# Performance work log

Measured on AMD Instinct MI355X. Metric: run time of the kernel, lower is better.

The kernel has to match this reference:

```python
import jax, jax.numpy as jnp
import numpy as np

BSZ, N, DEG = 32, 128, 8
HID, NODE_F, EDGE_F = 64, 32, 16
E_PER_G = N * DEG
E_TOT = BSZ * E_PER_G
N_TOT = BSZ * N


def _edges():
    # ring-style unique edges per graph: (i, (i+d) % N) for d in 1..DEG
    i = np.repeat(np.arange(N), DEG)              # [N*DEG]
    d = np.tile(np.arange(1, DEG + 1), N)
    src_l = np.tile(i, BSZ)                       # local src per edge
    dst_l = np.tile((i + d) % N, BSZ)
    off = np.repeat(np.arange(BSZ) * N, E_PER_G)
    ei = np.stack([src_l + off, dst_l + off])     # [2, E_TOT] global
    return jnp.asarray(ei, jnp.int32)


def setup_inputs() -> dict:
    key = jax.random.key(0)
    ks = jax.random.split(key, 16)
    def lin(k, fi, fo):
        s = 1.0 / np.sqrt(fi)
        kw, kb = jax.random.split(k)
        return (jax.random.uniform(kw, (fi, fo), jnp.float32, -s, s),
                jax.random.uniform(kb, (fo,), jnp.float32, -s, s))
    W_atom, b_atom = lin(ks[0], NODE_F, HID)
    W_bond, b_bond = lin(ks[1], EDGE_F, HID)
    be_w1, be_b1 = lin(ks[2], HID, HID)   # GINE bond_encoder MLP
    be_w2, be_b2 = lin(ks[3], HID, HID)
    nn_w1, nn_b1 = lin(ks[4], HID, HID)   # GINE update seq
    nn_w2, nn_b2 = lin(ks[5], HID, HID)
    m_w1, m_b1 = lin(ks[6], 2 * HID, HID) # final MLP: outer(HID)+edge(HID) -> HID -> 1
    m_w2, m_b2 = lin(ks[7], HID, 1)
    return {
        "x": jax.random.normal(ks[8], (N_TOT, NODE_F), jnp.float32),
        "edge_attr": jax.random.normal(ks[9], (E_TOT, EDGE_F), jnp.float32),
        "edge_index": _edges(),
        "batch": jnp.repeat(jnp.arange(BSZ, dtype=jnp.int32), N),
        "W_atom": W_atom, "b_atom": b_atom, "W_bond": W_bond, "b_bond": b_bond,
        "be_w1": be_w1, "be_b1": be_b1, "be_w2": be_w2, "be_b2": be_b2,
        "nn_w1": nn_w1, "nn_b1": nn_b1, "nn_w2": nn_w2, "nn_b2": nn_b2,
        "m_w1": m_w1, "m_b1": m_b1, "m_w2": m_w2, "m_b2": m_b2,
    }


def reference(x, edge_attr, edge_index, batch,
              W_atom, b_atom, W_bond, b_bond,
              be_w1, be_b1, be_w2, be_b2,
              nn_w1, nn_b1, nn_w2, nn_b2,
              m_w1, m_b1, m_w2, m_b2):
    src, dst = edge_index[0], edge_index[1]
    h = x @ W_atom + b_atom                                   # atom encoder [N_TOT, HID]
    e = edge_attr @ W_bond + b_bond                           # bond encoder [E_TOT, HID]
    # --- GINEConv (eps=0): nn(h + sum_j relu(h_j + mlp(e_ij))) ---
    ee = jax.nn.relu(e @ be_w1 + be_b1) @ be_w2 + be_b2
    msg = jax.nn.relu(h[src] + ee)
    agg = jax.ops.segment_sum(msg, dst, num_segments=N_TOT)
    h = jax.nn.relu((h + agg) @ nn_w1 + nn_b1) @ nn_w2 + nn_b2
    # --- dense batch (equal-size graphs -> exact reshape) ---
    logits = h.reshape(BSZ, N, HID)
    real_mask = jnp.ones((BSZ, N, N), dtype=bool)
    # --- outer pairwise tuples ---
    outer = jnp.einsum('bnk,bmk->bnmk', logits, logits)       # [B,N,N,HID]
    # --- scatter edge embeddings into dense [B,N,N,HID] ---
    g = src // N
    ls, ld = src % N, dst % N
    dense_e = jnp.zeros((BSZ, N, N, HID), e.dtype).at[g, ls, ld].set(e)
    emb = jnp.concatenate([outer, dense_e], axis=-1)          # [B,N,N,2*HID]
    emb = jax.nn.relu(emb @ m_w1 + m_b1) @ m_w2 + m_b2        # [B,N,N,1]
    return emb, real_mask
```

## Files before the change

kernel.cpp:

```cpp
#include <hip/hip_runtime.h>

#define BSZ 32
#define NN 128
#define DEG 8
#define HID 64
#define NODE_F 32
#define EDGE_F 16
#define E_PER_G (NN * DEG)
#define E_TOT (BSZ * E_PER_G)
#define N_TOT (BSZ * NN)
#define EMB_SIZE (BSZ * NN * NN)

typedef __attribute__((ext_vector_type(8))) short short8;
typedef __attribute__((ext_vector_type(4))) float f32x4;

__device__ __forceinline__ unsigned short f2bf(float f) {
    unsigned u = __builtin_bit_cast(unsigned, f);
    u += 0x7FFF + ((u >> 16) & 1);
    return (unsigned short)(u >> 16);
}
__device__ __forceinline__ float bf2f(unsigned short s) {
    unsigned u = ((unsigned)s) << 16;
    return __builtin_bit_cast(float, u);
}
__device__ __forceinline__ int lds_b(int row, int col) {
    return row * 128 + (((col >> 3) ^ (row & 7)) << 4) + ((col & 7) << 1);
}
__device__ __forceinline__ int lds_c(int row, int c8) {
    return row * 128 + ((c8 ^ (row & 7)) << 4);
}

__global__ __launch_bounds__(256) void k_pre(const float* __restrict__ x,
        const float* __restrict__ W_atom, const float* __restrict__ b_atom,
        const float* __restrict__ W_bond, const float* __restrict__ be_w1,
        const float* __restrict__ be_w2, const float* __restrict__ m_w1,
        const float* __restrict__ nn_w1, const float* __restrict__ nn_w2,
        float* __restrict__ h, unsigned short* __restrict__ PK,
        unsigned short* __restrict__ W1T) {
    int tid = threadIdx.x;
    if (blockIdx.x < 256) {
        __shared__ float xs[16][NODE_F];
        int i2 = tid * 2;
        float2 v = *(const float2*)&x[(size_t)blockIdx.x * 16 * NODE_F + i2];
        xs[i2 >> 5][i2 & 31] = v.x;
        xs[i2 >> 5][(i2 & 31) + 1] = v.y;
        int j = tid & 63, q = tid >> 6;
        float ww[NODE_F];
#pragma unroll
        for (int k = 0; k < NODE_F; ++k) ww[k] = W_atom[k * HID + j];
        float bj = b_atom[j];
        __syncthreads();
#pragma unroll
        for (int r = 0; r < 4; ++r) {
            int row = q * 4 + r;
            float acc = bj;
#pragma unroll
            for (int k = 0; k < NODE_F; ++k) acc = fmaf(xs[row][k], ww[k], acc);
            h[(size_t)(blockIdx.x * 16 + row) * HID + j] = acc;
        }
    } else {
        int t = (blockIdx.x - 256) * 256 + tid;
        int m = t >> 12;
        int idx = t & 4095;
        if (m < 6) {
            int i = idx & 7, lr = (idx >> 3) & 15, lg = (idx >> 7) & 3;
            int jt = (idx >> 9) & 3, kh = (idx >> 11) & 1;
            int k = kh * 32 + lg * 8 + i, j = jt * 16 + lr;
            float v;
            switch (m) {
                case 0:  v = (k < EDGE_F) ? W_bond[k * HID + j] : 0.f; break;
                case 1:  v = be_w1[k * HID + j]; break;
                case 2:  v = be_w2[k * HID + j]; break;
                case 3:  v = m_w1[(HID + k) * HID + j]; break;
                case 4:  v = nn_w1[k * HID + j]; break;
                default: v = nn_w2[k * HID + j]; break;
            }
            PK[m * 4096 + idx] = f2bf(v);
        } else {
            int j = idx >> 6, k = idx & 63;
            W1T[idx] = f2bf(m_w1[k * HID + j]);
        }
    }
}

__global__ __launch_bounds__(256) void k_edgeM(
        const float* __restrict__ ea, const float* __restrict__ h,
        const float* __restrict__ b_bond, const float* __restrict__ be_b1,
        const float* __restrict__ be_b2, const unsigned short* __restrict__ PK,
        float* __restrict__ E1, unsigned short* __restrict__ msgb) {
    __shared__ char ebuf[64 * 128];
    __shared__ char tbuf[64 * 128];
    int tid = threadIdx.x;
    int w = tid >> 6, l = tid & 63, lr = l & 15, lg = l >> 4;
    int e0 = blockIdx.x * 64;
    int R0 = w * 16;

    short8 af = (short8){0, 0, 0, 0, 0, 0, 0, 0};
    if (lg < 2) {
        const float* p = ea + (size_t)(e0 + R0 + lr) * EDGE_F + lg * 8;
        float4 x0 = *(const float4*)p;
        float4 x1 = *(const float4*)(p + 4);
        af[0] = (short)f2bf(x0.x); af[1] = (short)f2bf(x0.y);
        af[2] = (short)f2bf(x0.z); af[3] = (short)f2bf(x0.w);
        af[4] = (short)f2bf(x1.x); af[5] = (short)f2bf(x1.y);
        af[6] = (short)f2bf(x1.z); af[7] = (short)f2bf(x1.w);
    }
    f32x4 a0[4];
#pragma unroll
    for (int jt = 0; jt < 4; ++jt) a0[jt] = (f32x4){0.f, 0.f, 0.f, 0.f};
#pragma unroll
    for (int jt = 0; jt < 4; ++jt) {
        short8 bw = *(const short8*)(PK + 0 * 4096 + (size_t)(((0 * 4 + jt) * 4 + lg) * 16 + lr) * 8);
        a0[jt] = __builtin_amdgcn_mfma_f32_16x16x32_bf16(af, bw, a0[jt], 0, 0, 0);
    }
#pragma unroll
    for (int jt = 0; jt < 4; ++jt) {
        float bb = b_bond[jt * 16 + lr];
#pragma unroll
        for (int r = 0; r < 4; ++r) {
            int row = R0 + lg * 4 + r, col = jt * 16 + lr;
            *(unsigned short*)(ebuf + lds_b(row, col)) = f2bf(a0[jt][r] + bb);
        }
    }
    short8 ae[2];
#pragma unroll
    for (int kh = 0; kh < 2; ++kh)
        ae[kh] = *(const short8*)(ebuf + lds_c(R0 + lr, kh * 4 + lg));
    f32x4 a1[4];
#pragma unroll
    for (int jt = 0; jt < 4; ++jt) a1[jt] = (f32x4){0.f, 0.f, 0.f, 0.f};
#pragma unroll
    for (int kh = 0; kh < 2; ++kh)
#pragma unroll
        for (int jt = 0; jt < 4; ++jt) {
            short8 bw = *(const short8*)(PK + 3 * 4096 + (size_t)(((kh * 4 + jt) * 4 + lg) * 16 + lr) * 8);
            a1[jt] = __builtin_amdgcn_mfma_f32_16x16x32_bf16(ae[kh], bw, a1[jt], 0, 0, 0);
        }
#pragma unroll
    for (int jt = 0; jt < 4; ++jt)
        *(f32x4*)(E1 + (size_t)(e0 + R0) * HID + jt * 256 + l * 4) = a1[jt];
    f32x4 a2[4];
#pragma unroll
    for (int jt = 0; jt < 4; ++jt) a2[jt] = (f32x4){0.f, 0.f, 0.f, 0.f};
#pragma unroll
    for (int kh = 0; kh < 2; ++kh)
#pragma unroll
        for (int jt = 0; jt < 4; ++jt) {
            short8 bw = *(const short8*)(PK + 1 * 4096 + (size_t)(((kh * 4 + jt) * 4 + lg) * 16 + lr) * 8);
            a2[jt] = __builtin_amdgcn_mfma_f32_16x16x32_bf16(ae[kh], bw, a2[jt], 0, 0, 0);
        }
#pragma unroll
    for (int jt = 0; jt < 4; ++jt) {
        float b1j = be_b1[jt * 16 + lr];
#pragma unroll
        for (int r = 0; r < 4; ++r) {
            int row = R0 + lg * 4 + r, col = jt * 16 + lr;
            *(unsigned short*)(tbuf + lds_b(row, col)) = f2bf(fmaxf(a2[jt][r] + b1j, 0.f));
        }
    }
    short8 at[2];
#pragma unroll
    for (int kh = 0; kh < 2; ++kh)
        at[kh] = *(const short8*)(tbuf + lds_c(R0 + lr, kh * 4 + lg));
    f32x4 a3[4];
#pragma unroll
    for (int jt = 0; jt < 4; ++jt) a3[jt] = (f32x4){0.f, 0.f, 0.f, 0.f};
#pragma unroll
    for (int kh = 0; kh < 2; ++kh)
#pragma unroll
        for (int jt = 0; jt < 4; ++jt) {
            short8 bw = *(const short8*)(PK + 2 * 4096 + (size_t)(((kh * 4 + jt) * 4 + lg) * 16 + lr) * 8);
            a3[jt] = __builtin_amdgcn_mfma_f32_16x16x32_bf16(at[kh], bw, a3[jt], 0, 0, 0);
        }
    int g = e0 >> 10;
#pragma unroll
    for (int jt = 0; jt < 4; ++jt) {
        float b2j = be_b2[jt * 16 + lr];
#pragma unroll
        for (int r = 0; r < 4; ++r) {
            int row = R0 + lg * 4 + r;
            int ig = (e0 & 1023) + row;
            int src = g * NN + (ig >> 3);
            float hv = h[(size_t)src * HID + jt * 16 + lr];
            float mv = fmaxf(hv + a3[jt][r] + b2j, 0.f);
            msgb[(size_t)(e0 + row) * HID + jt * 16 + lr] = f2bf(mv);
        }
    }
}

__global__ __launch_bounds__(128) void k_nodeM(
        const float* __restrict__ h, const unsigned short* __restrict__ msgb,
        const float* __restrict__ nb1, const float* __restrict__ nb2,
        const unsigned short* __restrict__ PK, unsigned short* __restrict__ Lbf) {
    __shared__ char ub[16 * 128];
    __shared__ char tb[16 * 128];
    int tid = threadIdx.x;
    int n0 = blockIdx.x * 16;
    int g = n0 >> 7, nl0 = n0 & 127;
    {
        int r = tid >> 3;
        int c0 = (tid & 7) * 8;
        int nl = nl0 + r;
        float u[8];
        float4 h0 = *(const float4*)&h[(size_t)(n0 + r) * HID + c0];
        float4 h1 = *(const float4*)&h[(size_t)(n0 + r) * HID + c0 + 4];
        u[0] = h0.x; u[1] = h0.y; u[2] = h0.z; u[3] = h0.w;
        u[4] = h1.x; u[5] = h1.y; u[6] = h1.z; u[7] = h1.w;
#pragma unroll
        for (int d = 1; d <= 8; ++d) {
            int eid = g * E_PER_G + ((nl - d) & 127) * DEG + (d - 1);
            uint4 mv = *(const uint4*)&msgb[(size_t)eid * HID + c0];
            unsigned wd[4] = {mv.x, mv.y, mv.z, mv.w};
#pragma unroll
            for (int q = 0; q < 4; ++q) {
                u[q * 2]     += bf2f((unsigned short)(wd[q] & 0xffff));
                u[q * 2 + 1] += bf2f((unsigned short)(wd[q] >> 16));
            }
        }
        uint4 pk;
        pk.x = (unsigned)f2bf(u[0]) | ((unsigned)f2bf(u[1]) << 16);
        pk.y = (unsigned)f2bf(u[2]) | ((unsigned)f2bf(u[3]) << 16);
        pk.z = (unsigned)f2bf(u[4]) | ((unsigned)f2bf(u[5]) << 16);
        pk.w = (unsigned)f2bf(u[6]) | ((unsigned)f2bf(u[7]) << 16);
        *(uint4*)(ub + lds_c(r, tid & 7)) = pk;
    }
    __syncthreads();
    int w = tid >> 6, l = tid & 63, lr = l & 15, lg = l >> 4;
    short8 au[2];
#pragma unroll
    for (int kh = 0; kh < 2; ++kh)
        au[kh] = *(const short8*)(ub + lds_c(lr, kh * 4 + lg));
    f32x4 a1[2];
#pragma unroll
    for (int q = 0; q < 2; ++q) a1[q] = (f32x4){0.f, 0.f, 0.f, 0.f};
#pragma unroll
    for (int q = 0; q < 2; ++q) {
        int jt = w * 2 + q;
#pragma unroll
        for (int kh = 0; kh < 2; ++kh) {
            short8 bw = *(const short8*)(PK + 4 * 4096 + (size_t)(((kh * 4 + jt) * 4 + lg) * 16 + lr) * 8);
            a1[q] = __builtin_amdgcn_mfma_f32_16x16x32_bf16(au[kh], bw, a1[q], 0, 0, 0);
        }
    }
#pragma unroll
    for (int q = 0; q < 2; ++q) {
        int jt = w * 2 + q;
        float b1j = nb1[jt * 16 + lr];
#pragma unroll
        for (int r = 0; r < 4; ++r) {
            int row = lg * 4 + r, col = jt * 16 + lr;
            *(unsigned short*)(tb + lds_b(row, col)) = f2bf(fmaxf(a1[q][r] + b1j, 0.f));
        }
    }
    __syncthreads();
    short8 at[2];
#pragma unroll
    for (int kh = 0; kh < 2; ++kh)
        at[kh] = *(const short8*)(tb + lds_c(lr, kh * 4 + lg));
    f32x4 a2[2];
#pragma unroll
    for (int q = 0; q < 2; ++q) a2[q] = (f32x4){0.f, 0.f, 0.f, 0.f};
#pragma unroll
    for (int q = 0; q < 2; ++q) {
        int jt = w * 2 + q;
#pragma unroll
        for (int kh = 0; kh < 2; ++kh) {
            short8 bw = *(const short8*)(PK + 5 * 4096 + (size_t)(((kh * 4 + jt) * 4 + lg) * 16 + lr) * 8);
            a2[q] = __builtin_amdgcn_mfma_f32_16x16x32_bf16(at[kh], bw, a2[q], 0, 0, 0);
        }
    }
#pragma unroll
    for (int q = 0; q < 2; ++q) {
        int jt = w * 2 + q;
        float b2j = nb2[jt * 16 + lr];
#pragma unroll
        for (int r = 0; r < 4; ++r) {
            int row = lg * 4 + r;
            Lbf[(size_t)(n0 + row) * HID + jt * 16 + lr] = f2bf(a2[q][r] + b2j);
        }
    }
}

__global__ __launch_bounds__(256, 4) void k_pair(
        const unsigned short* __restrict__ Lbf, const float* __restrict__ E1,
        const unsigned short* __restrict__ W1T,
        const float* __restrict__ m_b1, const float* __restrict__ m_w2,
        const float* __restrict__ m_b2, float* __restrict__ out,
        float* __restrict__ mask, int write_mask) {
    __shared__ uint4 Ls[1024];
    __shared__ float eseg[1024];
    int tid = threadIdx.x;
    int bid = (blockIdx.x & 7) * 256 + (blockIdx.x >> 3);
    int b = bid >> 6;
    int nb = (bid & 63) * 2;
    if (write_mask && tid < 64) {
        *(float4*)(mask + (size_t)(b * NN + nb) * NN + tid * 4) =
            make_float4(1.f, 1.f, 1.f, 1.f);
    }
    const uint4* src = (const uint4*)(Lbf + (size_t)b * NN * HID);
#pragma unroll
    for (int it = 0; it < 4; ++it) {
        int i = it * 256 + tid;
        int row = i >> 3, c = i & 7;
        Ls[(row << 3) | (c ^ (row & 7))] = src[i];
    }
    ((float4*)eseg)[tid] = ((const float4*)(E1 + (size_t)(b * E_PER_G + nb * DEG) * HID))[tid];

    int w = tid >> 6, l = tid & 63, lr = l & 15, lg = l >> 4;
    int n = nb + (w >> 1);
    int hm = (w & 1) * 64;
    const unsigned short* LnG = Lbf + (size_t)(b * NN + n) * HID;
    short8 an[2][4];
#pragma unroll
    for (int kh = 0; kh < 2; ++kh) {
        short8 lnc = *(const short8*)(LnG + kh * 32 + lg * 8);
        float lf[8];
#pragma unroll
        for (int i = 0; i < 8; ++i) lf[i] = bf2f((unsigned short)lnc[i]);
#pragma unroll
        for (int jt = 0; jt < 4; ++jt) {
            short8 w1t = *(const short8*)(W1T + (size_t)(jt * 16 + lr) * HID + kh * 32 + lg * 8);
#pragma unroll
            for (int i = 0; i < 8; ++i)
                an[kh][jt][i] = (short)f2bf(lf[i] * bf2f((unsigned short)w1t[i]));
        }
    }
    float4 b1v[4], w2v[4];
#pragma unroll
    for (int jt = 0; jt < 4; ++jt) {
        b1v[jt] = *(const float4*)&m_b1[jt * 16 + lg * 4];
        w2v[jt] = *(const float4*)&m_w2[jt * 16 + lg * 4];
    }
    float bias2 = m_b2[0];
    __syncthreads();

    const unsigned short* Lsu = (const unsigned short*)Ls;
    float* orow = out + ((size_t)(b * NN + n)) * NN;
#pragma unroll
    for (int mt = 0; mt < 4; ++mt) {
        int row = hm + mt * 16 + lr;
        f32x4 acc[4];
#pragma unroll
        for (int jt = 0; jt < 4; ++jt) acc[jt] = (f32x4){0.f, 0.f, 0.f, 0.f};
#pragma unroll
        for (int kh = 0; kh < 2; ++kh) {
            int c = kh * 4 + lg;
            short8 afr = *(const short8*)(Lsu + (size_t)((row << 3) | (c ^ (row & 7))) * 8);
#pragma unroll
            for (int jt = 0; jt < 4; ++jt)
                acc[jt] = __builtin_amdgcn_mfma_f32_16x16x32_bf16(an[kh][jt], afr, acc[jt], 0, 0, 0);
        }
        int m = row;
        int d = (m - n) & 127;
        bool has_e = (unsigned)(d - 1) < 8u;
        float s = 0.f;
        if (has_e) {
            int rowin = (w >> 1) * 8 + (d - 1);
            int base = (rowin >> 2) * 64 + (rowin & 3);
#pragma unroll
            for (int jt = 0; jt < 4; ++jt) {
                int o = jt * 256 + base + lg * 16;
                float e0v = eseg[o +  0];
                float e1v = eseg[o +  4];
                float e2v = eseg[o +  8];
                float e3v = eseg[o + 12];
                s = fmaf(fmaxf(acc[jt][0] + b1v[jt].x + e0v, 0.f), w2v[jt].x, s);
                s = fmaf(fmaxf(acc[jt][1] + b1v[jt].y + e1v, 0.f), w2v[jt].y, s);
                s = fmaf(fmaxf(acc[jt][2] + b1v[jt].z + e2v, 0.f), w2v[jt].z, s);
                s = fmaf(fmaxf(acc[jt][3] + b1v[jt].w + e3v, 0.f), w2v[jt].w, s);
            }
        } else {
#pragma unroll
            for (int jt = 0; jt < 4; ++jt) {
                s = fmaf(fmaxf(acc[jt][0] + b1v[jt].x, 0.f), w2v[jt].x, s);
                s = fmaf(fmaxf(acc[jt][1] + b1v[jt].y, 0.f), w2v[jt].y, s);
                s = fmaf(fmaxf(acc[jt][2] + b1v[jt].z, 0.f), w2v[jt].z, s);
                s = fmaf(fmaxf(acc[jt][3] + b1v[jt].w, 0.f), w2v[jt].w, s);
            }
        }
        s += __shfl_xor(s, 16);
        s += __shfl_xor(s, 32);
        if (lg == 0) orow[m] = s + bias2;
    }
}

extern "C" void kernel_launch(void* const* d_in, const int* in_sizes, int n_in,
                              void* d_out, int out_size, void* d_ws, size_t ws_size,
                              hipStream_t stream) {
    const float* x         = (const float*)d_in[0];
    const float* edge_attr = (const float*)d_in[1];
    const float* W_atom = (const float*)d_in[4];
    const float* b_atom = (const float*)d_in[5];
    const float* W_bond = (const float*)d_in[6];
    const float* b_bond = (const float*)d_in[7];
    const float* be_w1  = (const float*)d_in[8];
    const float* be_b1  = (const float*)d_in[9];
    const float* be_w2  = (const float*)d_in[10];
    const float* be_b2  = (const float*)d_in[11];
    const float* nn_w1  = (const float*)d_in[12];
    const float* nn_b1  = (const float*)d_in[13];
    const float* nn_w2  = (const float*)d_in[14];
    const float* nn_b2  = (const float*)d_in[15];
    const float* m_w1   = (const float*)d_in[16];
    const float* m_b1   = (const float*)d_in[17];
    const float* m_w2   = (const float*)d_in[18];
    const float* m_b2   = (const float*)d_in[19];

    char* ws = (char*)d_ws;
    float* h   = (float*)ws;                   ws += (size_t)N_TOT * HID * 4;
    float* E1  = (float*)ws;                   ws += (size_t)E_TOT * HID * 4;
    unsigned short* msgb = (unsigned short*)ws; ws += (size_t)E_TOT * HID * 2;
    unsigned short* Lbf  = (unsigned short*)ws; ws += (size_t)N_TOT * HID * 2;
    unsigned short* W1T  = (unsigned short*)ws; ws += (size_t)HID * HID * 2;
    unsigned short* PK   = (unsigned short*)ws; ws += (size_t)6 * 4096 * 2;

    k_pre<<<256 + 112, 256, 0, stream>>>(x, W_atom, b_atom, W_bond, be_w1, be_w2,
                                         m_w1, nn_w1, nn_w2, h, PK, W1T);
    k_edgeM<<<E_TOT / 64, 256, 0, stream>>>(edge_attr, h, b_bond, be_b1, be_b2,
                                            PK, E1, msgb);
    k_nodeM<<<N_TOT / 16, 128, 0, stream>>>(h, msgb, nn_b1, nn_b2, PK, Lbf);

    float* out = (float*)d_out;
    float* mask = out + EMB_SIZE;
    int write_mask = (out_size >= 2 * EMB_SIZE) ? 1 : 0;
    k_pair<<<BSZ * 64, 256, 0, stream>>>(Lbf, E1, W1T, m_b1, m_w2, m_b2,
                                         out, mask, write_mask);
}
```

Before: 41.74 us.

## Fuse edge message and node update kernels into one per-graph kernel

Merges the edge-MLP kernel and the node-aggregation/update kernel into a single kernel with one 512-thread block per graph. Messages are kept in LDS (128 KB) instead of being written to and reread from a global bf16 buffer, and one kernel launch is removed. In exchange, the grid shrinks to 32 blocks, so most CUs sit idle and each block loops serially over 8 edge tiles.

```diff
diff --git a/kernel.cpp b/kernel.cpp
--- a/kernel.cpp
+++ b/kernel.cpp
@@ -22,6 +22,9 @@
 __device__ __forceinline__ float bf2f(unsigned short s) {
     unsigned u = ((unsigned)s) << 16;
     return __builtin_bit_cast(float, u);
+}
+__device__ __forceinline__ unsigned pk2(float a, float b) {
+    return (unsigned)f2bf(a) | ((unsigned)f2bf(b) << 16);
 }
 __device__ __forceinline__ int lds_b(int row, int col) {
     return row * 128 + (((col >> 3) ^ (row & 7)) << 4) + ((col & 7) << 1);
@@ -83,200 +86,187 @@
     }
 }
 
-__global__ __launch_bounds__(256) void k_edgeM(
+__global__ __launch_bounds__(512) void k_graph(
         const float* __restrict__ ea, const float* __restrict__ h,
         const float* __restrict__ b_bond, const float* __restrict__ be_b1,
-        const float* __restrict__ be_b2, const unsigned short* __restrict__ PK,
-        float* __restrict__ E1, unsigned short* __restrict__ msgb) {
-    __shared__ char ebuf[64 * 128];
-    __shared__ char tbuf[64 * 128];
+        const float* __restrict__ be_b2,
+        const float* __restrict__ nb1, const float* __restrict__ nb2,
+        const unsigned short* __restrict__ PK,
+        float* __restrict__ E1, unsigned short* __restrict__ Lbf) {
+    __shared__ char msgL[E_PER_G * 128];
+    __shared__ char wbuf[8][2048];
     int tid = threadIdx.x;
+    int g = blockIdx.x;
     int w = tid >> 6, l = tid & 63, lr = l & 15, lg = l >> 4;
-    int e0 = blockIdx.x * 64;
-    int R0 = w * 16;
-
-    short8 af = (short8){0, 0, 0, 0, 0, 0, 0, 0};
-    if (lg < 2) {
-        const float* p = ea + (size_t)(e0 + R0 + lr) * EDGE_F + lg * 8;
-        float4 x0 = *(const float4*)p;
-        float4 x1 = *(const float4*)(p + 4);
-        af[0] = (short)f2bf(x0.x); af[1] = (short)f2bf(x0.y);
-        af[2] = (short)f2bf(x0.z); af[3] = (short)f2bf(x0.w);
-        af[4] = (short)f2bf(x1.x); af[5] = (short)f2bf(x1.y);
-        af[6] = (short)f2bf(x1.z); af[7] = (short)f2bf(x1.w);
-    }
-    f32x4 a0[4];
-#pragma unroll
-    for (int jt = 0; jt < 4; ++jt) a0[jt] = (f32x4){0.f, 0.f, 0.f, 0.f};
-#pragma unroll
-    for (int jt = 0; jt < 4; ++jt) {
-        short8 bw = *(const short8*)(PK + 0 * 4096 + (size_t)(((0 * 4 + jt) * 4 + lg) * 16 + lr) * 8);
-        a0[jt] = __builtin_amdgcn_mfma_f32_16x16x32_bf16(af, bw, a0[jt], 0, 0, 0);
-    }
-#pragma unroll
-    for (int jt = 0; jt < 4; ++jt) {
-        float bb = b_bond[jt * 16 + lr];
-#pragma unroll
-        for (int r = 0; r < 4; ++r) {
-            int row = R0 + lg * 4 + r, col = jt * 16 + lr;
-            *(unsigned short*)(ebuf + lds_b(row, col)) = f2bf(a0[jt][r] + bb);
-        }
-    }
-    short8 ae[2];
-#pragma unroll
-    for (int kh = 0; kh < 2; ++kh)
-        ae[kh] = *(const short8*)(ebuf + lds_c(R0 + lr, kh * 4 + lg));
-    f32x4 a1[4];
-#pragma unroll
-    for (int jt = 0; jt < 4; ++jt) a1[jt] = (f32x4){0.f, 0.f, 0.f, 0.f};
-#pragma unroll
-    for (int kh = 0; kh < 2; ++kh)
-#pragma unroll
-        for (int jt = 0; jt < 4; ++jt) {
-            short8 bw = *(const short8*)(PK + 3 * 4096 + (size_t)(((kh * 4 + jt) * 4 + lg) * 16 + lr) * 8);
-            a1[jt] = __builtin_amdgcn_mfma_f32_16x16x32_bf16(ae[kh], bw, a1[jt], 0, 0, 0);
-        }
-#pragma unroll
-    for (int jt = 0; jt < 4; ++jt)
-        *(f32x4*)(E1 + (size_t)(e0 + R0) * HID + jt * 256 + l * 4) = a1[jt];
-    f32x4 a2[4];
-#pragma unroll
-    for (int jt = 0; jt < 4; ++jt) a2[jt] = (f32x4){0.f, 0.f, 0.f, 0.f};
-#pragma unroll
-    for (int kh = 0; kh < 2; ++kh)
-#pragma unroll
-        for (int jt = 0; jt < 4; ++jt) {
-            short8 bw = *(const short8*)(PK + 1 * 4096 + (size_t)(((kh * 4 + jt) * 4 + lg) * 16 + lr) * 8);
-            a2[jt] = __builtin_amdgcn_mfma_f32_16x16x32_bf16(ae[kh], bw, a2[jt], 0, 0, 0);
-        }
-#pragma unroll
-    for (int jt = 0; jt < 4; ++jt) {
-        float b1j = be_b1[jt * 16 + lr];
-#pragma unroll
-        for (int r = 0; r < 4; ++r) {
-            int row = R0 + lg * 4 + r, col = jt * 16 + lr;
-            *(unsigned short*)(tbuf + lds_b(row, col)) = f2bf(fmaxf(a2[jt][r] + b1j, 0.f));
-        }
-    }
-    short8 at[2];
-#pragma unroll
-    for (int kh = 0; kh < 2; ++kh)
-        at[kh] = *(const short8*)(tbuf + lds_c(R0 + lr, kh * 4 + lg));
-    f32x4 a3[4];
-#pragma unroll
-    for (int jt = 0; jt < 4; ++jt) a3[jt] = (f32x4){0.f, 0.f, 0.f, 0.f};
-#pragma unroll
-    for (int kh = 0; kh < 2; ++kh)
-#pragma unroll
-        for (int jt = 0; jt < 4; ++jt) {
-            short8 bw = *(const short8*)(PK + 2 * 4096 + (size_t)(((kh * 4 + jt) * 4 + lg) * 16 + lr) * 8);
-            a3[jt] = __builtin_amdgcn_mfma_f32_16x16x32_bf16(at[kh], bw, a3[jt], 0, 0, 0);
-        }
-    int g = e0 >> 10;
-#pragma unroll
-    for (int jt = 0; jt < 4; ++jt) {
-        float b2j = be_b2[jt * 16 + lr];
-#pragma unroll
-        for (int r = 0; r < 4; ++r) {
-            int row = R0 + lg * 4 + r;
-            int ig = (e0 & 1023) + row;
-            int src = g * NN + (ig >> 3);
-            float hv = h[(size_t)src * HID + jt * 16 + lr];
-            float mv = fmaxf(hv + a3[jt][r] + b2j, 0.f);
-            msgb[(size_t)(e0 + row) * HID + jt * 16 + lr] = f2bf(mv);
-        }
-    }
-}
-
-__global__ __launch_bounds__(128) void k_nodeM(
-        const float* __restrict__ h, const unsigned short* __restrict__ msgb,
-        const float* __restrict__ nb1, const float* __restrict__ nb2,
-        const unsigned short* __restrict__ PK, unsigned short* __restrict__ Lbf) {
-    __shared__ char ub[16 * 128];
-    __shared__ char tb[16 * 128];
-    int tid = threadIdx.x;
-    int n0 = blockIdx.x * 16;
-    int g = n0 >> 7, nl0 = n0 & 127;
+    char* wb = wbuf[w];
+
+#pragma unroll 1
+    for (int it = 0; it < 8; ++it) {
+        int ebase = it * 128 + w * 16;
+        int eid0 = g * E_PER_G + ebase;
+        short8 af = (short8){0, 0, 0, 0, 0, 0, 0, 0};
+        if (lg < 2) {
+            const float* p = ea + (size_t)(eid0 + lr) * EDGE_F + lg * 8;
+            float4 x0 = *(const float4*)p;
+            float4 x1 = *(const float4*)(p + 4);
+            af[0] = (short)f2bf(x0.x); af[1] = (short)f2bf(x0.y);
+            af[2] = (short)f2bf(x0.z); af[3] = (short)f2bf(x0.w);
+            af[4] = (short)f2bf(x1.x); af[5] = (short)f2bf(x1.y);
+            af[6] = (short)f2bf(x1.z); af[7] = (short)f2bf(x1.w);
+        }
+        f32x4 a0[4];
+#pragma unroll
+        for (int jt = 0; jt < 4; ++jt) a0[jt] = (f32x4){0.f, 0.f, 0.f, 0.f};
+#pragma unroll
+        for (int jt = 0; jt < 4; ++jt) {
+            short8 bw = *(const short8*)(PK + 0 * 4096 + (size_t)((jt * 4 + lg) * 16 + lr) * 8);
+            a0[jt] = __builtin_amdgcn_mfma_f32_16x16x32_bf16(af, bw, a0[jt], 0, 0, 0);
+        }
+#pragma unroll
+        for (int jt = 0; jt < 4; ++jt) {
+            float bb = b_bond[jt * 16 + lr];
+#pragma unroll
+            for (int r = 0; r < 4; ++r)
+                *(unsigned short*)(wb + lds_b(lg * 4 + r, jt * 16 + lr)) = f2bf(a0[jt][r] + bb);
+        }
+        short8 ae[2];
+#pragma unroll
+        for (int kh = 0; kh < 2; ++kh)
+            ae[kh] = *(const short8*)(wb + lds_c(lr, kh * 4 + lg));
+        f32x4 a1[4];
+#pragma unroll
+        for (int jt = 0; jt < 4; ++jt) a1[jt] = (f32x4){0.f, 0.f, 0.f, 0.f};
+#pragma unroll
+        for (int kh = 0; kh < 2; ++kh)
+#pragma unroll
+            for (int jt = 0; jt < 4; ++jt) {
+                short8 bw = *(const short8*)(PK + 3 * 4096 + (size_t)(((kh * 4 + jt) * 4 + lg) * 16 + lr) * 8);
+                a1[jt] = __builtin_amdgcn_mfma_f32_16x16x32_bf16(ae[kh], bw, a1[jt], 0, 0, 0);
+            }
+#pragma unroll
+        for (int jt = 0; jt < 4; ++jt)
+            *(f32x4*)(E1 + (size_t)eid0 * HID + jt * 256 + l * 4) = a1[jt];
+        f32x4 a2[4];
+#pragma unroll
+        for (int jt = 0; jt < 4; ++jt) a2[jt] = (f32x4){0.f, 0.f, 0.f, 0.f};
+#pragma unroll
+        for (int kh = 0; kh < 2; ++kh)
+#pragma unroll
+            for (int jt = 0; jt < 4; ++jt) {
+                short8 bw = *(const short8*)(PK + 1 * 4096 + (size_t)(((kh * 4 + jt) * 4 + lg) * 16 + lr) * 8);
+                a2[jt] = __builtin_amdgcn_mfma_f32_16x16x32_bf16(ae[kh], bw, a2[jt], 0, 0, 0);
+            }
+#pragma unroll
+        for (int jt = 0; jt < 4; ++jt) {
+            float b1j = be_b1[jt * 16 + lr];
+#pragma unroll
+            for (int r = 0; r < 4; ++r)
+                *(unsigned short*)(wb + lds_b(lg * 4 + r, jt * 16 + lr)) = f2bf(fmaxf(a2[jt][r] + b1j, 0.f));
+        }
+        short8 at[2];
+#pragma unroll
+        for (int kh = 0; kh < 2; ++kh)
+            at[kh] = *(const short8*)(wb + lds_c(lr, kh * 4 + lg));
+        f32x4 a3[4];
+#pragma unroll
+        for (int jt = 0; jt < 4; ++jt) a3[jt] = (f32x4){0.f, 0.f, 0.f, 0.f};
+#pragma unroll
+        for (int kh = 0; kh < 2; ++kh)
+#pragma unroll
+            for (int jt = 0; jt < 4; ++jt) {
+                short8 bw = *(const short8*)(PK + 2 * 4096 + (size_t)(((kh * 4 + jt) * 4 + lg) * 16 + lr) * 8);
+                a3[jt] = __builtin_amdgcn_mfma_f32_16x16x32_bf16(at[kh], bw, a3[jt], 0, 0, 0);
+            }
+#pragma unroll
+        for (int jt = 0; jt < 4; ++jt) {
+            float b2j = be_b2[jt * 16 + lr];
+#pragma unroll
+            for (int r = 0; r < 4; ++r) {
+                int grow = ebase + lg * 4 + r;
+                int src = grow >> 3;
+                float hv = h[(size_t)(g * NN + src) * HID + jt * 16 + lr];
+                float mv = fmaxf(hv + a3[jt][r] + b2j, 0.f);
+                *(unsigned short*)(msgL + lds_b(grow, jt * 16 + lr)) = f2bf(mv);
+            }
+        }
+    }
+    __syncthreads();
+
     {
-        int r = tid >> 3;
-        int c0 = (tid & 7) * 8;
-        int nl = nl0 + r;
-        float u[8];
-        float4 h0 = *(const float4*)&h[(size_t)(n0 + r) * HID + c0];
-        float4 h1 = *(const float4*)&h[(size_t)(n0 + r) * HID + c0 + 4];
-        u[0] = h0.x; u[1] = h0.y; u[2] = h0.z; u[3] = h0.w;
-        u[4] = h1.x; u[5] = h1.y; u[6] = h1.z; u[7] = h1.w;
+        int nl = tid >> 2;
+        int c0 = (tid & 3) * 16;
+        int j0 = c0 >> 3;
+        float u[16];
+        const float* hp = h + (size_t)(g * NN + nl) * HID + c0;
+#pragma unroll
+        for (int q = 0; q < 4; ++q) {
+            float4 hv = *(const float4*)(hp + q * 4);
+            u[q * 4 + 0] = hv.x; u[q * 4 + 1] = hv.y;
+            u[q * 4 + 2] = hv.z; u[q * 4 + 3] = hv.w;
+        }
 #pragma unroll
         for (int d = 1; d <= 8; ++d) {
-            int eid = g * E_PER_G + ((nl - d) & 127) * DEG + (d - 1);
-            uint4 mv = *(const uint4*)&msgb[(size_t)eid * HID + c0];
-            unsigned wd[4] = {mv.x, mv.y, mv.z, mv.w};
-#pragma unroll
-            for (int q = 0; q < 4; ++q) {
+            int row = ((nl - d) & 127) * DEG + (d - 1);
+            uint4 m0 = *(const uint4*)(msgL + lds_c(row, j0));
+            uint4 m1 = *(const uint4*)(msgL + lds_c(row, j0 + 1));
+            unsigned wd[8] = {m0.x, m0.y, m0.z, m0.w, m1.x, m1.y, m1.z, m1.w};
+#pragma unroll
+            for (int q = 0; q < 8; ++q) {
                 u[q * 2]     += bf2f((unsigned short)(wd[q] & 0xffff));
                 u[q * 2 + 1] += bf2f((unsigned short)(wd[q] >> 16));
             }
         }
-        uint4 pk;
-        pk.x = (unsigned)f2bf(u[0]) | ((unsigned)f2bf(u[1]) << 16);
-        pk.y = (unsigned)f2bf(u[2]) | ((unsigned)f2bf(u[3]) << 16);
-        pk.z = (unsigned)f2bf(u[4]) | ((unsigned)f2bf(u[5]) << 16);
-        pk.w = (unsigned)f2bf(u[6]) | ((unsigned)f2bf(u[7]) << 16);
-        *(uint4*)(ub + lds_c(r, tid & 7)) = pk;
-    }
-    __syncthreads();
-    int w = tid >> 6, l = tid & 63, lr = l & 15, lg = l >> 4;
+        int lrow = (tid >> 2) & 15;
+        uint4 A, B;
+        A.x = pk2(u[0], u[1]);  A.y = pk2(u[2], u[3]);
+        A.z = pk2(u[4], u[5]);  A.w = pk2(u[6], u[7]);
+        B.x = pk2(u[8], u[9]);  B.y = pk2(u[10], u[11]);
+        B.z = pk2(u[12], u[13]); B.w = pk2(u[14], u[15]);
+        *(uint4*)(wb + lds_c(lrow, j0)) = A;
+        *(uint4*)(wb + lds_c(lrow, j0 + 1)) = B;
+    }
     short8 au[2];
 #pragma unroll
     for (int kh = 0; kh < 2; ++kh)
-        au[kh] = *(const short8*)(ub + lds_c(lr, kh * 4 + lg));
-    f32x4 a1[2];
-#pragma unroll
-    for (int q = 0; q < 2; ++q) a1[q] = (f32x4){0.f, 0.f, 0.f, 0.f};
-#pragma unroll
-    for (int q = 0; q < 2; ++q) {
-        int jt = w * 2 + q;
-#pragma unroll
-        for (int kh = 0; kh < 2; ++kh) {
+        au[kh] = *(const short8*)(wb + lds_c(lr, kh * 4 + lg));
+    f32x4 c1[4];
+#pragma unroll
+    for (int jt = 0; jt < 4; ++jt) c1[jt] = (f32x4){0.f, 0.f, 0.f, 0.f};
+#pragma unroll
+    for (int kh = 0; kh < 2; ++kh)
+#pragma unroll
+        for (int jt = 0; jt < 4; ++jt) {
             short8 bw = *(const short8*)(PK + 4 * 4096 + (size_t)(((kh * 4 + jt) * 4 + lg) * 16 + lr) * 8);
-            a1[q] = __builtin_amdgcn_mfma_f32_16x16x32_bf16(au[kh], bw, a1[q], 0, 0, 0);
-        }
-    }
-#pragma unroll
-    for (int q = 0; q < 2; ++q) {
-        int jt = w * 2 + q;
+            c1[jt] = __builtin_amdgcn_mfma_f32_16x16x32_bf16(au[kh], bw, c1[jt], 0, 0, 0);
+        }
+#pragma unroll
+    for (int jt = 0; jt < 4; ++jt) {
         float b1j = nb1[jt * 16 + lr];
 #pragma unroll
+        for (int r = 0; r < 4; ++r)
+            *(unsigned short*)(wb + lds_b(lg * 4 + r, jt * 16 + lr)) = f2bf(fmaxf(c1[jt][r] + b1j, 0.f));
+    }
+    short8 at2[2];
+#pragma unroll
+    for (int kh = 0; kh < 2; ++kh)
+        at2[kh] = *(const short8*)(wb + lds_c(lr, kh * 4 + lg));
+    f32x4 c2[4];
+#pragma unroll
+    for (int jt = 0; jt < 4; ++jt) c2[jt] = (f32x4){0.f, 0.f, 0.f, 0.f};
+#pragma unroll
+    for (int kh = 0; kh < 2; ++kh)
+#pragma unroll
+        for (int jt = 0; jt < 4; ++jt) {
+            short8 bw = *(const short8*)(PK + 5 * 4096 + (size_t)(((kh * 4 + jt) * 4 + lg) * 16 + lr) * 8);
+            c2[jt] = __builtin_amdgcn_mfma_f32_16x16x32_bf16(at2[kh], bw, c2[jt], 0, 0, 0);
+        }
+#pragma unroll
+    for (int jt = 0; jt < 4; ++jt) {
+        float b2j = nb2[jt * 16 + lr];
+#pragma unroll
         for (int r = 0; r < 4; ++r) {
-            int row = lg * 4 + r, col = jt * 16 + lr;
-            *(unsigned short*)(tb + lds_b(row, col)) = f2bf(fmaxf(a1[q][r] + b1j, 0.f));
-        }
-    }
-    __syncthreads();
-    short8 at[2];
-#pragma unroll
-    for (int kh = 0; kh < 2; ++kh)
-        at[kh] = *(const short8*)(tb + lds_c(lr, kh * 4 + lg));
-    f32x4 a2[2];
-#pragma unroll
-    for (int q = 0; q < 2; ++q) a2[q] = (f32x4){0.f, 0.f, 0.f, 0.f};
-#pragma unroll
-    for (int q = 0; q < 2; ++q) {
-        int jt = w * 2 + q;
-#pragma unroll
-        for (int kh = 0; kh < 2; ++kh) {
-            short8 bw = *(const short8*)(PK + 5 * 4096 + (size_t)(((kh * 4 + jt) * 4 + lg) * 16 + lr) * 8);
-            a2[q] = __builtin_amdgcn_mfma_f32_16x16x32_bf16(at[kh], bw, a2[q], 0, 0, 0);
-        }
-    }
-#pragma unroll
-    for (int q = 0; q < 2; ++q) {
-        int jt = w * 2 + q;
-        float b2j = nb2[jt * 16 + lr];
-#pragma unroll
-        for (int r = 0; r < 4; ++r) {
-            int row = lg * 4 + r;
-            Lbf[(size_t)(n0 + row) * HID + jt * 16 + lr] = f2bf(a2[q][r] + b2j);
+            int node = w * 16 + lg * 4 + r;
+            Lbf[(size_t)(g * NN + node) * HID + jt * 16 + lr] = f2bf(c2[jt][r] + b2j);
         }
     }
 }
@@ -409,16 +399,14 @@
     char* ws = (char*)d_ws;
     float* h   = (float*)ws;                   ws += (size_t)N_TOT * HID * 4;
     float* E1  = (float*)ws;                   ws += (size_t)E_TOT * HID * 4;
-    unsigned short* msgb = (unsigned short*)ws; ws += (size_t)E_TOT * HID * 2;
     unsigned short* Lbf  = (unsigned short*)ws; ws += (size_t)N_TOT * HID * 2;
     unsigned short* W1T  = (unsigned short*)ws; ws += (size_t)HID * HID * 2;
     unsigned short* PK   = (unsigned short*)ws; ws += (size_t)6 * 4096 * 2;
 
     k_pre<<<256 + 112, 256, 0, stream>>>(x, W_atom, b_atom, W_bond, be_w1, be_w2,
                                          m_w1, nn_w1, nn_w2, h, PK, W1T);
-    k_edgeM<<<E_TOT / 64, 256, 0, stream>>>(edge_attr, h, b_bond, be_b1, be_b2,
-                                            PK, E1, msgb);
-    k_nodeM<<<N_TOT / 16, 128, 0, stream>>>(h, msgb, nn_b1, nn_b2, PK, Lbf);
+    k_graph<<<BSZ, 512, 0, stream>>>(edge_attr, h, b_bond, be_b1, be_b2,
+                                     nn_b1, nn_b2, PK, E1, Lbf);
 
     float* out = (float*)d_out;
     float* mask = out + EMB_SIZE;
```

New measurement: 48.92 us. 1.17x slower.
